# Kernel tuning notes

Measured on AMD Instinct MI355X. Metric: run time of the kernel, lower is better.

Reference implementation:

```python
import jax, jax.numpy as jnp
import numpy as np
import math

B, SQ, SKV, D = 16, 1024, 1024, 256


def setup_inputs() -> dict:
    key = jax.random.key(0)
    kq, kk, kv, km = jax.random.split(key, 4)
    # Scale inputs down: the module applies exp() to raw QK^T logits, so dot
    # products must stay small to avoid overflow (std ~ 0.05^2*sqrt(D) ~ 0.04).
    scale = 0.05
    query = jax.random.normal(kq, (B, SQ, D), dtype=jnp.float32) * scale
    key_t = jax.random.normal(kk, (B, SKV, D), dtype=jnp.float32) * scale
    value = jax.random.normal(kv, (B, SKV, D), dtype=jnp.float32)
    mask = jax.random.randint(km, (B, SQ, SKV), 0, 2, dtype=jnp.int32)
    return {"query": query, "key": key_t, "value": value, "mask": mask}


def reference(query, key, value, mask):
    # scores = exp(Q K^T) / sqrt(d)  -- note: exp BEFORE scaling, as in source
    d = query.shape[-1]
    inv_sqrt_d = jnp.float32(1.0 / math.sqrt(d))
    scores = jnp.exp(jnp.einsum('bqd,bkd->bqk', query, key)) * inv_sqrt_d
    # masked_fill(mask == 0, -1e9)
    scores = jnp.where(mask == 0, jnp.float32(-1e9), scores)
    p_attn = jax.nn.softmax(scores, axis=-1)
    # dropout is identity in eval mode (deterministic reference)
    output = jnp.einsum('bqk,bkd->bqd', p_attn, value)
    # flatten=True path: sum over the query/sequence dim
    return output.sum(axis=1), p_attn
```

## Files before the change

kernel.cpp:

```cpp
#include <hip/hip_runtime.h>

#define NB   16
#define NSQ  1024
#define NSKV 1024
#define ND   256

typedef __bf16    bf16x8 __attribute__((ext_vector_type(8)));
typedef float     f32x4  __attribute__((ext_vector_type(4)));
typedef _Float16  f16x4  __attribute__((ext_vector_type(4)));

#define EST 268

__global__ __launch_bounds__(256) void prep_kernel(
    const float* __restrict__ K, __bf16* __restrict__ Kbf,
    const int* __restrict__ mask, unsigned* __restrict__ mw,
    float* __restrict__ colsum, float* __restrict__ out0)
{
    const int bid = blockIdx.x;
    const int tid = threadIdx.x;
    if (bid < 2048) {
        const int i    = bid * 256 + tid;
        const int lane = i & 63;
        const int m    = lane & 15;
        const int kg   = lane >> 4;
        const int dc   = (i >> 6) & 7;
        const int kvb  = (i >> 9) & 63;
        const int b    = i >> 15;
        const float* s = K + ((size_t)(b * NSKV + kvb * 16 + m)) * ND + dc * 32 + kg * 8;
        float4 a = *(const float4*)s;
        float4 c = *(const float4*)(s + 4);
        bf16x8 o;
        o[0] = (__bf16)a.x; o[1] = (__bf16)a.y; o[2] = (__bf16)a.z; o[3] = (__bf16)a.w;
        o[4] = (__bf16)c.x; o[5] = (__bf16)c.y; o[6] = (__bf16)c.z; o[7] = (__bf16)c.w;
        ((bf16x8*)Kbf)[i] = o;
    } else if (bid < 2048 + 4096) {
        const int row = (bid - 2048) * 4 + (tid >> 6);
        const int l   = tid & 63;
        const int4* mrow = (const int4*)(mask + (size_t)row * NSKV) + l * 4;
        unsigned w = 0;
        #pragma unroll
        for (int v = 0; v < 4; ++v) {
            int4 mv = mrow[v];
            w |= (mv.x != 0 ? 1u : 0u) << (v * 4 + 0);
            w |= (mv.y != 0 ? 1u : 0u) << (v * 4 + 1);
            w |= (mv.z != 0 ? 1u : 0u) << (v * 4 + 2);
            w |= (mv.w != 0 ? 1u : 0u) << (v * 4 + 3);
        }
        const int m    = l & 15;
        const int base = l & 48;
        unsigned out = 0;
        #pragma unroll
        for (int c = 0; c < 16; ++c) {
            unsigned v = (unsigned)__shfl((int)w, base | c);
            out |= ((v >> m) & 1u) << c;
        }
        mw[(size_t)row * 64 + l] = out;
    } else if (bid < 2048 + 4096 + 64) {
        colsum[(bid - 6144) * 256 + tid] = 0.f;
    } else {
        out0[(bid - 6208) * 256 + tid] = 0.f;
    }
}

__global__ __launch_bounds__(256, 4) void attn_fused(
    const float* __restrict__ Q, const __bf16* __restrict__ Kbf,
    const unsigned* __restrict__ mw, float* __restrict__ out_p,
    float* __restrict__ colsum)
{
    const int g    = blockIdx.x;
    const int tile = ((g & 7) << 7) | (g >> 3);
    const int b    = tile >> 6;
    const int q0   = (tile & 63) * 16;
    const int tid  = threadIdx.x;
    const int lane = tid & 63;
    const int h    = tid >> 6;
    const int m    = lane & 15;
    const int kg   = lane >> 4;

    __shared__ __attribute__((aligned(16))) _Float16 epark[4][16 * EST];
    __shared__ float Zs[4][16];
    __shared__ float invZs[16];

    _Float16* myE = &epark[h][0];

    bf16x8 afrag[8];
    {
        const float* qbase = Q + ((size_t)(b * NSQ + q0 + m)) * ND;
        #pragma unroll
        for (int dc = 0; dc < 8; ++dc) {
            const float* p4 = qbase + dc * 32 + kg * 8;
            float4 x = *(const float4*)(p4);
            float4 y = *(const float4*)(p4 + 4);
            bf16x8 a;
            a[0] = (__bf16)x.x; a[1] = (__bf16)x.y; a[2] = (__bf16)x.z; a[3] = (__bf16)x.w;
            a[4] = (__bf16)y.x; a[5] = (__bf16)y.y; a[6] = (__bf16)y.z; a[7] = (__bf16)y.w;
            afrag[dc] = a;
        }
    }

    unsigned mword[4];
    #pragma unroll
    for (int i = 0; i < 4; ++i)
        mword[i] = mw[(size_t)(b * NSQ + q0 + kg * 4 + i) * 64 + h * 16 + m];

    const bf16x8* kf = (const bf16x8*)Kbf + ((size_t)(b * 64 + h * 16) * 8) * 64 + lane;

    float zacc[4] = {0.f, 0.f, 0.f, 0.f};
    bf16x8 fA[8], fB[8];

    #define LDFRAG(gr, c) { \
        _Pragma("unroll") \
        for (int dc = 0; dc < 8; ++dc) \
            (gr)[dc] = kf[((c) * 8 + dc) * 64]; }

    #define COMPUTE(gr, c) { \
        f32x4 acc = {0.f, 0.f, 0.f, 0.f}; \
        _Pragma("unroll") \
        for (int dc = 0; dc < 8; ++dc) \
            acc = __builtin_amdgcn_mfma_f32_16x16x32_bf16(afrag[dc], (gr)[dc], acc, 0, 0, 0); \
        _Pragma("unroll") \
        for (int i = 0; i < 4; ++i) { \
            float e = ((mword[i] >> (c)) & 1u) ? __expf(__expf(acc[i]) * 0.0625f) : 0.f; \
            zacc[i] += e; \
            myE[(kg * 4 + i) * EST + (c) * 16 + m] = (_Float16)e; \
        } }

    LDFRAG(fA, 0);
    __builtin_amdgcn_sched_barrier(0);

    #pragma unroll
    for (int cc = 0; cc < 16; cc += 2) {
        LDFRAG(fB, cc + 1);
        __builtin_amdgcn_sched_barrier(0);
        COMPUTE(fA, cc);
        if (cc + 2 < 16) LDFRAG(fA, cc + 2);
        __builtin_amdgcn_sched_barrier(0);
        COMPUTE(fB, cc + 1);
    }
    #undef LDFRAG
    #undef COMPUTE

    #pragma unroll
    for (int i = 0; i < 4; ++i) {
        float z = zacc[i];
        z += __shfl_xor(z, 1);
        z += __shfl_xor(z, 2);
        z += __shfl_xor(z, 4);
        z += __shfl_xor(z, 8);
        if (m == 0) Zs[h][kg * 4 + i] = z;
    }
    __syncthreads();
    if (tid < 16)
        invZs[tid] = 1.0f / (Zs[0][tid] + Zs[1][tid] + Zs[2][tid] + Zs[3][tid]);
    __syncthreads();

    float csum[4] = {0.f, 0.f, 0.f, 0.f};
    float* prow = out_p + (size_t)(b * NSQ + q0) * NSKV + h * 256 + lane * 4;
    #pragma unroll
    for (int s = 0; s < 16; ++s) {
        f16x4 ev = *(const f16x4*)&myE[s * EST + lane * 4];
        const float iz = invZs[s];
        float4 pv;
        pv.x = (float)ev[0] * iz; pv.y = (float)ev[1] * iz;
        pv.z = (float)ev[2] * iz; pv.w = (float)ev[3] * iz;
        *(float4*)(prow + (size_t)s * NSKV) = pv;
        csum[0] += pv.x; csum[1] += pv.y; csum[2] += pv.z; csum[3] += pv.w;
    }
    #pragma unroll
    for (int j = 0; j < 4; ++j)
        atomicAdd(&colsum[b * NSKV + h * 256 + lane * 4 + j], csum[j]);
}

__global__ __launch_bounds__(256) void attn_out_kernel(
    const float* __restrict__ colsum, const float* __restrict__ V,
    float* __restrict__ out)
{
    const int b  = blockIdx.x >> 6;
    const int ks = (blockIdx.x & 63) << 4;
    const int d  = threadIdx.x;
    float acc = 0.f;
    #pragma unroll
    for (int k = 0; k < 16; ++k) {
        acc += colsum[b * NSKV + ks + k] * V[((size_t)(b * NSKV + ks + k)) * ND + d];
    }
    atomicAdd(&out[b * ND + d], acc);
}

extern "C" void kernel_launch(void* const* d_in, const int* in_sizes, int n_in,
                              void* d_out, int out_size, void* d_ws, size_t ws_size,
                              hipStream_t stream)
{
    (void)in_sizes; (void)n_in; (void)out_size; (void)ws_size;
    const float* Q    = (const float*)d_in[0];
    const float* K    = (const float*)d_in[1];
    const float* V    = (const float*)d_in[2];
    const int*   mask = (const int*)d_in[3];

    float* out0 = (float*)d_out;
    float* p    = out0 + NB * ND;

    float*    colsum = (float*)d_ws;
    __bf16*   Kbf    = (__bf16*)((char*)d_ws + (64 << 10));
    unsigned* mwbits = (unsigned*)((char*)d_ws + (64 << 10) + (size_t)NB * NSKV * ND * 2);

    prep_kernel<<<6224, 256, 0, stream>>>(K, Kbf, mask, mwbits, colsum, out0);
    attn_fused<<<NB * 64, 256, 0, stream>>>(Q, Kbf, mwbits, p, colsum);
    attn_out_kernel<<<NB * 64, 256, 0, stream>>>(colsum, V, out0);
}
```

Baseline: 208.1 us.

## Quantize Q and K to fp8 and use fp8 MFMA with asm-pipelined loads

Converts K (in prep) and Q (in the attention kernel) to fp8 instead of bf16 and switches the QK^T matmul to fp8 MFMA instructions. The K layout is repacked into 16-byte chunks, and loads go through inline-asm dwordx4 with explicit vmcnt waits for double buffering. This halves K storage and load traffic and the register footprint. It risks accuracy loss, since fp8 e4m3 has little precision for the small scaled logits.

```diff
diff --git a/kernel.cpp b/kernel.cpp
--- a/kernel.cpp
+++ b/kernel.cpp
@@ -5,14 +5,20 @@
 #define NSKV 1024
 #define ND   256
 
-typedef __bf16    bf16x8 __attribute__((ext_vector_type(8)));
 typedef float     f32x4  __attribute__((ext_vector_type(4)));
 typedef _Float16  f16x4  __attribute__((ext_vector_type(4)));
+typedef int       i32x4  __attribute__((ext_vector_type(4)));
+typedef long      lng2   __attribute__((ext_vector_type(2)));
 
 #define EST 268
 
+template<bool HI>
+__device__ __forceinline__ int pk_fp8(float a, float b, int old) {
+    return __builtin_amdgcn_cvt_pk_fp8_f32(a, b, old, HI);
+}
+
 __global__ __launch_bounds__(256) void prep_kernel(
-    const float* __restrict__ K, __bf16* __restrict__ Kbf,
+    const float* __restrict__ K, unsigned char* __restrict__ Kb8,
     const int* __restrict__ mask, unsigned* __restrict__ mw,
     float* __restrict__ colsum, float* __restrict__ out0)
 {
@@ -29,10 +35,14 @@
         const float* s = K + ((size_t)(b * NSKV + kvb * 16 + m)) * ND + dc * 32 + kg * 8;
         float4 a = *(const float4*)s;
         float4 c = *(const float4*)(s + 4);
-        bf16x8 o;
-        o[0] = (__bf16)a.x; o[1] = (__bf16)a.y; o[2] = (__bf16)a.z; o[3] = (__bf16)a.w;
-        o[4] = (__bf16)c.x; o[5] = (__bf16)c.y; o[6] = (__bf16)c.z; o[7] = (__bf16)c.w;
-        ((bf16x8*)Kbf)[i] = o;
+        int lo = pk_fp8<false>(a.x, a.y, 0);
+        lo     = pk_fp8<true >(a.z, a.w, lo);
+        int hi = pk_fp8<false>(c.x, c.y, 0);
+        hi     = pk_fp8<true >(c.z, c.w, hi);
+        int2 w; w.x = lo; w.y = hi;
+        const size_t obyte = ((size_t)((b * 64 + kvb) * 4 + (dc >> 1))) * 1024
+                           + lane * 16 + (dc & 1) * 8;
+        *(int2*)(Kb8 + obyte) = w;
     } else if (bid < 2048 + 4096) {
         const int row = (bid - 2048) * 4 + (tid >> 6);
         const int l   = tid & 63;
@@ -63,7 +73,7 @@
 }
 
 __global__ __launch_bounds__(256, 4) void attn_fused(
-    const float* __restrict__ Q, const __bf16* __restrict__ Kbf,
+    const float* __restrict__ Q, const unsigned char* __restrict__ Kb8,
     const unsigned* __restrict__ mw, float* __restrict__ out_p,
     float* __restrict__ colsum)
 {
@@ -83,7 +93,7 @@
 
     _Float16* myE = &epark[h][0];
 
-    bf16x8 afrag[8];
+    long afrag[8];
     {
         const float* qbase = Q + ((size_t)(b * NSQ + q0 + m)) * ND;
         #pragma unroll
@@ -91,10 +101,11 @@
             const float* p4 = qbase + dc * 32 + kg * 8;
             float4 x = *(const float4*)(p4);
             float4 y = *(const float4*)(p4 + 4);
-            bf16x8 a;
-            a[0] = (__bf16)x.x; a[1] = (__bf16)x.y; a[2] = (__bf16)x.z; a[3] = (__bf16)x.w;
-            a[4] = (__bf16)y.x; a[5] = (__bf16)y.y; a[6] = (__bf16)y.z; a[7] = (__bf16)y.w;
-            afrag[dc] = a;
+            int lo = pk_fp8<false>(x.x, x.y, 0);
+            lo     = pk_fp8<true >(x.z, x.w, lo);
+            int hi = pk_fp8<false>(y.x, y.y, 0);
+            hi     = pk_fp8<true >(y.z, y.w, hi);
+            afrag[dc] = (long)(((unsigned long long)(unsigned)hi << 32) | (unsigned)lo);
         }
     }
 
@@ -103,21 +114,43 @@
     for (int i = 0; i < 4; ++i)
         mword[i] = mw[(size_t)(b * NSQ + q0 + kg * 4 + i) * 64 + h * 16 + m];
 
-    const bf16x8* kf = (const bf16x8*)Kbf + ((size_t)(b * 64 + h * 16) * 8) * 64 + lane;
+    const char* kbase = (const char*)Kb8
+                      + (size_t)(b * 64 + h * 16) * 4096 + lane * 16;
 
     float zacc[4] = {0.f, 0.f, 0.f, 0.f};
-    bf16x8 fA[8], fB[8];
-
-    #define LDFRAG(gr, c) { \
-        _Pragma("unroll") \
-        for (int dc = 0; dc < 8; ++dc) \
-            (gr)[dc] = kf[((c) * 8 + dc) * 64]; }
+    i32x4 fA[4], fB[4];
+
+    #define LD4(gr, c) { \
+        const char* _p0 = kbase + (size_t)(c) * 4096; \
+        asm volatile( \
+            "global_load_dwordx4 %0, %4, off\n\t" \
+            "global_load_dwordx4 %1, %4, off offset:1024\n\t" \
+            "global_load_dwordx4 %2, %4, off offset:2048\n\t" \
+            "global_load_dwordx4 %3, %4, off offset:3072" \
+            : "=&v"((gr)[0]), "=&v"((gr)[1]), "=&v"((gr)[2]), "=&v"((gr)[3]) \
+            : "v"(_p0) \
+            : "memory"); }
+
+    #define W4(gr) { \
+        asm volatile("s_waitcnt vmcnt(4)" \
+            : "+v"((gr)[0]), "+v"((gr)[1]), "+v"((gr)[2]), "+v"((gr)[3]) \
+            :: "memory"); \
+        __builtin_amdgcn_sched_barrier(0); }
+
+    #define W0(gr) { \
+        asm volatile("s_waitcnt vmcnt(0)" \
+            : "+v"((gr)[0]), "+v"((gr)[1]), "+v"((gr)[2]), "+v"((gr)[3]) \
+            :: "memory"); \
+        __builtin_amdgcn_sched_barrier(0); }
 
     #define COMPUTE(gr, c) { \
         f32x4 acc = {0.f, 0.f, 0.f, 0.f}; \
         _Pragma("unroll") \
-        for (int dc = 0; dc < 8; ++dc) \
-            acc = __builtin_amdgcn_mfma_f32_16x16x32_bf16(afrag[dc], (gr)[dc], acc, 0, 0, 0); \
+        for (int j = 0; j < 4; ++j) { \
+            lng2 p_ = __builtin_bit_cast(lng2, (gr)[j]); \
+            acc = __builtin_amdgcn_mfma_f32_16x16x32_fp8_fp8(afrag[2*j],   p_[0], acc, 0, 0, 0); \
+            acc = __builtin_amdgcn_mfma_f32_16x16x32_fp8_fp8(afrag[2*j+1], p_[1], acc, 0, 0, 0); \
+        } \
         _Pragma("unroll") \
         for (int i = 0; i < 4; ++i) { \
             float e = ((mword[i] >> (c)) & 1u) ? __expf(__expf(acc[i]) * 0.0625f) : 0.f; \
@@ -125,19 +158,21 @@
             myE[(kg * 4 + i) * EST + (c) * 16 + m] = (_Float16)e; \
         } }
 
-    LDFRAG(fA, 0);
-    __builtin_amdgcn_sched_barrier(0);
+    LD4(fA, 0);
+    LD4(fB, 1);
 
     #pragma unroll
     for (int cc = 0; cc < 16; cc += 2) {
-        LDFRAG(fB, cc + 1);
-        __builtin_amdgcn_sched_barrier(0);
+        W4(fA);
         COMPUTE(fA, cc);
-        if (cc + 2 < 16) LDFRAG(fA, cc + 2);
-        __builtin_amdgcn_sched_barrier(0);
+        if (cc + 2 < 16) LD4(fA, cc + 2);
+        if (cc + 2 < 16) { W4(fB); } else { W0(fB); }
         COMPUTE(fB, cc + 1);
-    }
-    #undef LDFRAG
+        if (cc + 3 < 16) LD4(fB, cc + 3);
+    }
+    #undef LD4
+    #undef W4
+    #undef W0
     #undef COMPUTE
 
     #pragma unroll
@@ -199,11 +234,11 @@
     float* out0 = (float*)d_out;
     float* p    = out0 + NB * ND;
 
-    float*    colsum = (float*)d_ws;
-    __bf16*   Kbf    = (__bf16*)((char*)d_ws + (64 << 10));
-    unsigned* mwbits = (unsigned*)((char*)d_ws + (64 << 10) + (size_t)NB * NSKV * ND * 2);
-
-    prep_kernel<<<6224, 256, 0, stream>>>(K, Kbf, mask, mwbits, colsum, out0);
-    attn_fused<<<NB * 64, 256, 0, stream>>>(Q, Kbf, mwbits, p, colsum);
+    float*         colsum = (float*)d_ws;
+    unsigned char* Kb8    = (unsigned char*)d_ws + (64 << 10);
+    unsigned*      mwbits = (unsigned*)((char*)d_ws + (64 << 10) + (size_t)NB * NSKV * ND);
+
+    prep_kernel<<<6224, 256, 0, stream>>>(K, Kb8, mask, mwbits, colsum, out0);
+    attn_fused<<<NB * 64, 256, 0, stream>>>(Q, Kb8, mwbits, p, colsum);
     attn_out_kernel<<<NB * 64, 256, 0, stream>>>(colsum, V, out0);
 }
```

New measurement: 194.6 us. -6.5%, faster.
